# Kernel tuning notes

Measured on AMD Instinct MI355X. Metric: run time of the kernel, lower is better.

The kernel has to match this reference:

```python
import jax, jax.numpy as jnp
import numpy as np

N_NODES = 50000
N_EDGES = 800000
D = 64           # node feature / hidden dim for all 5 GCN layers
NUM_GRAPHS = 512
FINAL_NEURON = 128
OUT_DIM = 1
NUM_LAYERS = 5


def setup_inputs() -> dict:
    key = jax.random.key(0)
    ks = jax.random.split(key, 20)
    inp = {}
    inp["x"] = jax.random.normal(ks[0], (N_NODES, D), dtype=jnp.float32)
    inp["edge_index"] = jax.random.randint(ks[1], (2, N_EDGES), 0, N_NODES)
    inp["batch"] = jnp.sort(jax.random.randint(ks[2], (N_NODES,), 0, NUM_GRAPHS))
    # GCNConv weights (Glorot-ish) and biases for 5 layers, all D->D
    for i in range(NUM_LAYERS):
        inp[f"W{i+1}"] = jax.random.normal(ks[3 + i], (D, D), dtype=jnp.float32) / np.sqrt(D)
        inp[f"b{i+1}"] = jnp.zeros((D,), dtype=jnp.float32)
    inp["fc1_W"] = jax.random.normal(ks[10], (D, FINAL_NEURON), dtype=jnp.float32) / np.sqrt(D)
    inp["fc1_b"] = jnp.zeros((FINAL_NEURON,), dtype=jnp.float32)
    inp["fc2_W"] = jax.random.normal(ks[11], (FINAL_NEURON, OUT_DIM), dtype=jnp.float32) / np.sqrt(FINAL_NEURON)
    inp["fc2_b"] = jnp.zeros((OUT_DIM,), dtype=jnp.float32)
    return inp


def _gcn_conv(h, src, dst, dinv, W, b):
    # PyG GCNConv: x' = D^{-1/2} (A + I) D^{-1/2} (h W) + b, deg includes self-loop
    hw = h @ W                                           # [N, D_out]
    norm_e = dinv[src] * dinv[dst]                       # [E]
    msg = hw[src] * norm_e[:, None]                      # gather + scale
    agg = jax.ops.segment_sum(msg, dst, num_segments=h.shape[0])
    agg = agg + (dinv * dinv)[:, None] * hw              # self-loop contribution
    return agg + b


def reference(x, edge_index, batch, W1, b1, W2, b2, W3, b3, W4, b4, W5, b5,
              fc1_W, fc1_b, fc2_W, fc2_b):
    src, dst = edge_index[0], edge_index[1]
    n = x.shape[0]
    # degree on A + I (in-degree at dst, plus 1 self-loop)
    deg = jax.ops.segment_sum(jnp.ones(src.shape[0], x.dtype), dst, num_segments=n) + 1.0
    dinv = jax.lax.rsqrt(deg)
    h = x
    for W, b in ((W1, b1), (W2, b2), (W3, b3), (W4, b4), (W5, b5)):
        h = jax.nn.relu(_gcn_conv(h, src, dst, dinv, W, b))
    # global_add_pool readout over graph ids
    g = jax.ops.segment_sum(h, batch, num_segments=NUM_GRAPHS)   # [G, D]
    g = jax.nn.relu(g @ fc1_W + fc1_b)
    return g @ fc2_W + fc2_b                                     # [G, 1]
```

## Files before the change

kernel.cpp:

```cpp
#include <hip/hip_runtime.h>
#include <hip/hip_fp16.h>

#define N_NODES 50000
#define N_EDGES 800000
#define D 64
#define NUM_GRAPHS 512
#define FINAL_NEURON 128
#define SCAN_NB ((N_NODES + 255) / 256)

#define BN 16
#define NB_GEMM (N_NODES / BN)
#define NB_EDGE ((N_EDGES + 255) / 256)
#define ZS 72
#define WS 72
#define WELEM (D * WS)

typedef unsigned short ushort_t;
typedef _Float16 f16;
typedef __attribute__((ext_vector_type(4))) _Float16 f16x4;
typedef __attribute__((ext_vector_type(8))) _Float16 f16x8;
typedef __attribute__((ext_vector_type(4))) float f32x4;

struct WPtrs { const float* w[5]; };

__device__ __forceinline__ float2 h2f(unsigned v) {
    __half2 h = *reinterpret_cast<__half2*>(&v);
    return __half22float2(h);
}

__device__ __forceinline__ void acc_add8(float4& a0, float4& a1, uint4 u) {
    float2 p;
    p = h2f(u.x); a0.x += p.x; a0.y += p.y;
    p = h2f(u.y); a0.z += p.x; a0.w += p.y;
    p = h2f(u.z); a1.x += p.x; a1.y += p.y;
    p = h2f(u.w); a1.z += p.x; a1.w += p.y;
}

__global__ void k_zero_prep(int* cnt, WPtrs wp, f16* __restrict__ whi, f16* __restrict__ wlo) {
    int b = blockIdx.x;
    if (b < SCAN_NB) {
        int i = b * 256 + threadIdx.x;
        if (i < N_NODES) cnt[i] = 0;
        return;
    }
    int l = b - SCAN_NB;
    const float* W = wp.w[l];
    f16* hi = whi + l * WELEM;
    f16* lo = wlo + l * WELEM;
    for (int idx = threadIdx.x; idx < D * D; idx += 256) {
        int k = idx >> 6, j = idx & 63;
        float w = W[idx];
        f16 h = (f16)w;
        hi[j * WS + k] = h;
        lo[j * WS + k] = (f16)(w - (float)h);
    }
}

__global__ void k_hist(const int* __restrict__ dst, int* cnt, ushort_t* __restrict__ epos) {
    int e = blockIdx.x * blockDim.x + threadIdx.x;
    if (e < N_EDGES) epos[e] = (ushort_t)atomicAdd(&cnt[dst[e]], 1);
}

__global__ void k_blocksum(const int* __restrict__ cnt, int* __restrict__ bsum,
                           float* __restrict__ dinv, float* __restrict__ g) {
    __shared__ int sdata[256];
    int t = threadIdx.x;
    int i = blockIdx.x * 256 + t;
    int v = (i < N_NODES) ? cnt[i] : 0;
    if (i < N_NODES) dinv[i] = rsqrtf((float)v + 1.0f);
    if (i < NUM_GRAPHS * D) g[i] = 0.f;
    sdata[t] = v;
    __syncthreads();
    for (int s = 128; s > 0; s >>= 1) {
        if (t < s) sdata[t] += sdata[t + s];
        __syncthreads();
    }
    if (t == 0) bsum[blockIdx.x] = sdata[0];
}

__global__ void k_scanbsum(const int* __restrict__ bsum, int* __restrict__ boff) {
    __shared__ int buf[256];
    int t = threadIdx.x;
    int v = (t < SCAN_NB) ? bsum[t] : 0;
    buf[t] = v;
    __syncthreads();
    for (int off = 1; off < 256; off <<= 1) {
        int a = (t >= off) ? buf[t - off] : 0;
        __syncthreads();
        buf[t] += a;
        __syncthreads();
    }
    if (t < SCAN_NB) boff[t] = buf[t] - v;
}

__global__ void k_localscan(const int* __restrict__ cnt, const int* __restrict__ boff,
                            int* __restrict__ row) {
    __shared__ int buf[256];
    int t = threadIdx.x;
    int i = blockIdx.x * 256 + t;
    int v = (i < N_NODES) ? cnt[i] : 0;
    buf[t] = v;
    __syncthreads();
    for (int off = 1; off < 256; off <<= 1) {
        int a = (t >= off) ? buf[t - off] : 0;
        __syncthreads();
        buf[t] += a;
        __syncthreads();
    }
    if (i < N_NODES) row[i] = boff[blockIdx.x] + buf[t] - v;
    if (i == 0) row[N_NODES] = N_EDGES;
}

__device__ __forceinline__ void stage_w_lds(const f16* __restrict__ whi_g,
                                            const f16* __restrict__ wlo_g,
                                            f16* WhiT, f16* WloT, int t) {
    const uint4* sh = (const uint4*)whi_g;
    const uint4* sl = (const uint4*)wlo_g;
    uint4* dh = (uint4*)WhiT;
    uint4* dl = (uint4*)WloT;
#pragma unroll 3
    for (int i = 0; i < 3; ++i) {
        int idx = t + i * 256;
        if (idx < WELEM / 8) { dh[idx] = sh[idx]; dl[idx] = sl[idx]; }
    }
}

__device__ __forceinline__ void gather_node16(const int* __restrict__ row,
                                              const ushort_t* __restrict__ esrc,
                                              const uint4* __restrict__ hp,
                                              int n, int g, int q, float4& a0, float4& a1) {
    int e = row[n] + g, e1 = row[n + 1];
    if (g == 0) acc_add8(a0, a1, hp[(size_t)n * 8 + q]);
    int i0 = __builtin_nontemporal_load(esrc + e);
    int i1 = __builtin_nontemporal_load(esrc + e + 2);
    int i2 = __builtin_nontemporal_load(esrc + e + 4);
    int i3 = __builtin_nontemporal_load(esrc + e + 6);
    while (e + 6 < e1) {
        uint4 u0 = hp[(size_t)i0 * 8 + q];
        uint4 u1 = hp[(size_t)i1 * 8 + q];
        uint4 u2 = hp[(size_t)i2 * 8 + q];
        uint4 u3 = hp[(size_t)i3 * 8 + q];
        e += 8;
        i0 = __builtin_nontemporal_load(esrc + e);
        i1 = __builtin_nontemporal_load(esrc + e + 2);
        i2 = __builtin_nontemporal_load(esrc + e + 4);
        i3 = __builtin_nontemporal_load(esrc + e + 6);
        acc_add8(a0, a1, u0); acc_add8(a0, a1, u1);
        acc_add8(a0, a1, u2); acc_add8(a0, a1, u3);
    }
    for (; e < e1; e += 2) {
        int s = __builtin_nontemporal_load(esrc + e);
        acc_add8(a0, a1, hp[(size_t)s * 8 + q]);
    }
}

__device__ __forceinline__ void gemm_16x64(f16* zsh, const f16* WhiT, const f16* WloT,
                                           const float* dinvsh, int t) {
    int w = t >> 6, l = t & 63;
    int cb = w * 16;
    int lr = l & 15, lg = l >> 4;
    f32x4 acc = {0.f, 0.f, 0.f, 0.f};
    f16x8 a0  = *(const f16x8*)&zsh[lr * ZS + lg * 8];
    f16x8 a1  = *(const f16x8*)&zsh[lr * ZS + 32 + lg * 8];
    f16x8 bh0 = *(const f16x8*)&WhiT[(cb + lr) * WS + lg * 8];
    f16x8 bl0 = *(const f16x8*)&WloT[(cb + lr) * WS + lg * 8];
    f16x8 bh1 = *(const f16x8*)&WhiT[(cb + lr) * WS + 32 + lg * 8];
    f16x8 bl1 = *(const f16x8*)&WloT[(cb + lr) * WS + 32 + lg * 8];
    acc = __builtin_amdgcn_mfma_f32_16x16x32_f16(a0, bh0, acc, 0, 0, 0);
    acc = __builtin_amdgcn_mfma_f32_16x16x32_f16(a0, bl0, acc, 0, 0, 0);
    acc = __builtin_amdgcn_mfma_f32_16x16x32_f16(a1, bh1, acc, 0, 0, 0);
    acc = __builtin_amdgcn_mfma_f32_16x16x32_f16(a1, bl1, acc, 0, 0, 0);
    __syncthreads();
#pragma unroll
    for (int r = 0; r < 4; ++r) {
        int rrow = lg * 4 + r;
        float s = dinvsh[rrow];
        zsh[rrow * ZS + cb + lr] = (f16)(acc[r] * s);
    }
}

__global__ __launch_bounds__(256, 6)
void k_transform0(const float* __restrict__ x, const float* __restrict__ dinv,
                  const f16* __restrict__ whi_g, const f16* __restrict__ wlo_g,
                  __half* __restrict__ hout,
                  const int* __restrict__ src, const int* __restrict__ dst,
                  const int* __restrict__ row, const ushort_t* __restrict__ epos,
                  ushort_t* __restrict__ esrc) {
    int t = threadIdx.x;
    if (blockIdx.x >= NB_GEMM) {
        int e = (blockIdx.x - NB_GEMM) * 256 + t;
        if (e < N_EDGES) esrc[row[dst[e]] + (int)epos[e]] = (ushort_t)src[e];
        return;
    }
    __shared__ __attribute__((aligned(16))) f16 WhiT[WELEM];
    __shared__ __attribute__((aligned(16))) f16 WloT[WELEM];
    __shared__ __attribute__((aligned(16))) f16 zsh[BN * ZS];
    __shared__ float dinvsh[BN];
    int base = blockIdx.x * BN;
    stage_w_lds(whi_g, wlo_g, WhiT, WloT, t);
    if (t < BN) dinvsh[t] = dinv[base + t];

    int nl = t >> 4, c4 = t & 15;
    float4 xv = ((const float4*)x)[(size_t)(base + nl) * 16 + c4];
    f16x4 zv = {(f16)xv.x, (f16)xv.y, (f16)xv.z, (f16)xv.w};
    *(f16x4*)&zsh[nl * ZS + c4 * 4] = zv;
    __syncthreads();
    gemm_16x64(zsh, WhiT, WloT, dinvsh, t);
    __syncthreads();
    if (t < 128) {
        int n2 = t >> 3, q = t & 7;
        uint4 o = *(const uint4*)&zsh[n2 * ZS + q * 8];
        ((uint4*)hout)[(size_t)(base + n2) * 8 + q] = o;
    }
}

__global__ __launch_bounds__(256, 6)
void k_layer(const int* __restrict__ row, const ushort_t* __restrict__ esrc,
             const __half* __restrict__ hin, const float* __restrict__ dinv,
             const float* __restrict__ bias,
             const f16* __restrict__ whi_g, const f16* __restrict__ wlo_g,
             __half* __restrict__ hout) {
    __shared__ __attribute__((aligned(16))) f16 WhiT[WELEM];
    __shared__ __attribute__((aligned(16))) f16 WloT[WELEM];
    __shared__ __attribute__((aligned(16))) f16 zsh[BN * ZS];
    __shared__ float dinvsh[BN];
    int t = threadIdx.x;
    int base = blockIdx.x * BN;
    stage_w_lds(whi_g, wlo_g, WhiT, WloT, t);
    if (t < BN) dinvsh[t] = dinv[base + t];

    int nl = t >> 4, m = t & 15, g = m >> 3, q = m & 7;
    int n = base + nl;
    float4 a0 = {0,0,0,0}, a1 = {0,0,0,0};
    gather_node16(row, esrc, (const uint4*)hin, n, g, q, a0, a1);
    a0.x += __shfl_xor(a0.x, 8); a0.y += __shfl_xor(a0.y, 8);
    a0.z += __shfl_xor(a0.z, 8); a0.w += __shfl_xor(a0.w, 8);
    a1.x += __shfl_xor(a1.x, 8); a1.y += __shfl_xor(a1.y, 8);
    a1.z += __shfl_xor(a1.z, 8); a1.w += __shfl_xor(a1.w, 8);
    float s = dinv[n];
    float4 b0 = ((const float4*)bias)[2 * q];
    float4 b1 = ((const float4*)bias)[2 * q + 1];
    if (g == 0) {
        f16x8 zv;
        zv[0] = (f16)fmaxf(a0.x * s + b0.x, 0.f);
        zv[1] = (f16)fmaxf(a0.y * s + b0.y, 0.f);
        zv[2] = (f16)fmaxf(a0.z * s + b0.z, 0.f);
        zv[3] = (f16)fmaxf(a0.w * s + b0.w, 0.f);
        zv[4] = (f16)fmaxf(a1.x * s + b1.x, 0.f);
        zv[5] = (f16)fmaxf(a1.y * s + b1.y, 0.f);
        zv[6] = (f16)fmaxf(a1.z * s + b1.z, 0.f);
        zv[7] = (f16)fmaxf(a1.w * s + b1.w, 0.f);
        *(f16x8*)&zsh[nl * ZS + q * 8] = zv;
    }
    __syncthreads();
    gemm_16x64(zsh, WhiT, WloT, dinvsh, t);
    __syncthreads();
    if (t < 128) {
        int n2 = t >> 3, q2 = t & 7;
        uint4 o = *(const uint4*)&zsh[n2 * ZS + q2 * 8];
        ((uint4*)hout)[(size_t)(base + n2) * 8 + q2] = o;
    }
}

__global__ __launch_bounds__(256, 6)
void k_layer_pool(const int* __restrict__ row, const ushort_t* __restrict__ esrc,
                  const __half* __restrict__ hin, const float* __restrict__ dinv,
                  const float* __restrict__ bias, const int* __restrict__ batch,
                  float* __restrict__ g) {
    __shared__ float zf[BN * 68];
    __shared__ int bsh[BN];
    int t = threadIdx.x;
    int base = blockIdx.x * BN;
    if (t < BN) bsh[t] = batch[base + t];

    int nl = t >> 4, m = t & 15, g2 = m >> 3, q = m & 7;
    int n = base + nl;
    float4 a0 = {0,0,0,0}, a1 = {0,0,0,0};
    gather_node16(row, esrc, (const uint4*)hin, n, g2, q, a0, a1);
    a0.x += __shfl_xor(a0.x, 8); a0.y += __shfl_xor(a0.y, 8);
    a0.z += __shfl_xor(a0.z, 8); a0.w += __shfl_xor(a0.w, 8);
    a1.x += __shfl_xor(a1.x, 8); a1.y += __shfl_xor(a1.y, 8);
    a1.z += __shfl_xor(a1.z, 8); a1.w += __shfl_xor(a1.w, 8);
    float s = dinv[n];
    float4 b0 = ((const float4*)bias)[2 * q];
    float4 b1 = ((const float4*)bias)[2 * q + 1];
    if (g2 == 0) {
        float4 r0, r1;
        r0.x = fmaxf(a0.x * s + b0.x, 0.f);
        r0.y = fmaxf(a0.y * s + b0.y, 0.f);
        r0.z = fmaxf(a0.z * s + b0.z, 0.f);
        r0.w = fmaxf(a0.w * s + b0.w, 0.f);
        r1.x = fmaxf(a1.x * s + b1.x, 0.f);
        r1.y = fmaxf(a1.y * s + b1.y, 0.f);
        r1.z = fmaxf(a1.z * s + b1.z, 0.f);
        r1.w = fmaxf(a1.w * s + b1.w, 0.f);
        *(float4*)&zf[nl * 68 + q * 8]     = r0;
        *(float4*)&zf[nl * 68 + q * 8 + 4] = r1;
    }
    __syncthreads();
    int f = t & 63, grp = t >> 6;
    int n0 = grp * 4;
    int cur = bsh[n0];
    float acc = 0.f;
#pragma unroll
    for (int k2 = 0; k2 < 4; ++k2) {
        int bb = bsh[n0 + k2];
        if (bb != cur) { atomicAdd(&g[cur * D + f], acc); acc = 0.f; cur = bb; }
        acc += zf[(n0 + k2) * 68 + f];
    }
    atomicAdd(&g[cur * D + f], acc);
}

__global__ void k_mlp(const float* __restrict__ g, const float* __restrict__ W1,
                      const float* __restrict__ b1, const float* __restrict__ W2,
                      const float* __restrict__ b2, float* __restrict__ out) {
    __shared__ float red[FINAL_NEURON];
    int row = blockIdx.x;
    int j = threadIdx.x;
    float acc = 0.f;
#pragma unroll
    for (int k = 0; k < D; ++k) acc += g[row * D + k] * W1[k * FINAL_NEURON + j];
    acc = fmaxf(acc + b1[j], 0.f);
    red[j] = acc * W2[j];
    __syncthreads();
    for (int s = 64; s > 0; s >>= 1) {
        if (j < s) red[j] += red[j + s];
        __syncthreads();
    }
    if (j == 0) out[row] = red[0] + b2[0];
}

extern "C" void kernel_launch(void* const* d_in, const int* in_sizes, int n_in,
                              void* d_out, int out_size, void* d_ws, size_t ws_size,
                              hipStream_t stream) {
    const float* x     = (const float*)d_in[0];
    const int*   ei    = (const int*)d_in[1];
    const int*   src   = ei;
    const int*   dst   = ei + N_EDGES;
    const int*   batch = (const int*)d_in[2];
    WPtrs wp;
    wp.w[0] = (const float*)d_in[3];  wp.w[1] = (const float*)d_in[5];
    wp.w[2] = (const float*)d_in[7];  wp.w[3] = (const float*)d_in[9];
    wp.w[4] = (const float*)d_in[11];
    const float* b[5]  = {(const float*)d_in[4], (const float*)d_in[6], (const float*)d_in[8],
                          (const float*)d_in[10], (const float*)d_in[12]};
    const float* fc1W  = (const float*)d_in[13];
    const float* fc1b  = (const float*)d_in[14];
    const float* fc2W  = (const float*)d_in[15];
    const float* fc2b  = (const float*)d_in[16];
    float* out = (float*)d_out;

    __half*   yA   = (__half*)d_ws;
    __half*   yB   = yA + (size_t)N_NODES * D;
    f16*      whiG = (f16*)(yB + (size_t)N_NODES * D);
    f16*      wloG = whiG + 5 * WELEM;
    float*    g    = (float*)(wloG + 5 * WELEM);
    float*    dinv = g + NUM_GRAPHS * D;
    int*      cnt  = (int*)(dinv + N_NODES);
    int*      row  = cnt + N_NODES;
    int*      bsum = row + N_NODES + 1;
    int*      boff = bsum + 256;
    ushort_t* epos = (ushort_t*)(boff + 256);
    ushort_t* esrc = epos + N_EDGES;

    k_zero_prep<<<SCAN_NB + 5, 256, 0, stream>>>(cnt, wp, whiG, wloG);
    k_hist<<<(N_EDGES + 255) / 256, 256, 0, stream>>>(dst, cnt, epos);
    k_blocksum<<<SCAN_NB, 256, 0, stream>>>(cnt, bsum, dinv, g);
    k_scanbsum<<<1, 256, 0, stream>>>(bsum, boff);
    k_localscan<<<SCAN_NB, 256, 0, stream>>>(cnt, boff, row);

    k_transform0<<<NB_GEMM + NB_EDGE, 256, 0, stream>>>(x, dinv, whiG, wloG, yA,
                                                        src, dst, row, epos, esrc);

    k_layer<<<NB_GEMM, 256, 0, stream>>>(row, esrc, yA, dinv, b[0],
                                         whiG + 1 * WELEM, wloG + 1 * WELEM, yB);
    k_layer<<<NB_GEMM, 256, 0, stream>>>(row, esrc, yB, dinv, b[1],
                                         whiG + 2 * WELEM, wloG + 2 * WELEM, yA);
    k_layer<<<NB_GEMM, 256, 0, stream>>>(row, esrc, yA, dinv, b[2],
                                         whiG + 3 * WELEM, wloG + 3 * WELEM, yB);
    k_layer<<<NB_GEMM, 256, 0, stream>>>(row, esrc, yB, dinv, b[3],
                                         whiG + 4 * WELEM, wloG + 4 * WELEM, yA);

    k_layer_pool<<<NB_GEMM, 256, 0, stream>>>(row, esrc, yA, dinv, b[4], batch, g);

    k_mlp<<<NUM_GRAPHS, FINAL_NEURON, 0, stream>>>(g, fc1W, fc1b, fc2W, fc2b, out);
}
```

Baseline: 262.8 us.

## Fuse transform, GCN layers, pooling and MLP into one cooperative persistent kernel

Merges the edge-scatter/first transform, four layer kernels, the pooled last layer and the MLP head into a single cooperative kernel. Blocks loop over tiles persistently and use grid-wide syncs between stages, replacing seven kernel launches and their inter-kernel gaps. Each block stages a layer's weights into LDS once per layer instead of once per tile. The trade-offs are grid-sync cost, a grid capped by occupancy (256 CUs assumed), and LDS reuse across stages. The edge scatter now runs before the transform inside the same blocks rather than in parallel blocks.

```diff
diff --git a/kernel.cpp b/kernel.cpp
--- a/kernel.cpp
+++ b/kernel.cpp
@@ -1,5 +1,8 @@
 #include <hip/hip_runtime.h>
 #include <hip/hip_fp16.h>
+#include <hip/hip_cooperative_groups.h>
+
+namespace cg = cooperative_groups;
 
 #define N_NODES 50000
 #define N_EDGES 800000
@@ -10,7 +13,7 @@
 
 #define BN 16
 #define NB_GEMM (N_NODES / BN)
-#define NB_EDGE ((N_EDGES + 255) / 256)
+#define NB_EDGE (N_EDGES / 256)
 #define ZS 72
 #define WS 72
 #define WELEM (D * WS)
@@ -22,6 +25,19 @@
 typedef __attribute__((ext_vector_type(4))) float f32x4;
 
 struct WPtrs { const float* w[5]; };
+
+struct MegaArgs {
+    const float* x;
+    const int* src; const int* dst; const int* batch;
+    const int* row; const ushort_t* epos; ushort_t* esrc;
+    const float* dinv;
+    const f16* whi[5]; const f16* wlo[5];
+    const float* bias[5];
+    __half* yA; __half* yB;
+    float* g;
+    const float* fc1W; const float* fc1b; const float* fc2W; const float* fc2b;
+    float* out;
+};
 
 __device__ __forceinline__ float2 h2f(unsigned v) {
     __half2 h = *reinterpret_cast<__half2*>(&v);
@@ -180,154 +196,152 @@
 }
 
 __global__ __launch_bounds__(256, 6)
-void k_transform0(const float* __restrict__ x, const float* __restrict__ dinv,
-                  const f16* __restrict__ whi_g, const f16* __restrict__ wlo_g,
-                  __half* __restrict__ hout,
-                  const int* __restrict__ src, const int* __restrict__ dst,
-                  const int* __restrict__ row, const ushort_t* __restrict__ epos,
-                  ushort_t* __restrict__ esrc) {
-    int t = threadIdx.x;
-    if (blockIdx.x >= NB_GEMM) {
-        int e = (blockIdx.x - NB_GEMM) * 256 + t;
-        if (e < N_EDGES) esrc[row[dst[e]] + (int)epos[e]] = (ushort_t)src[e];
-        return;
-    }
-    __shared__ __attribute__((aligned(16))) f16 WhiT[WELEM];
-    __shared__ __attribute__((aligned(16))) f16 WloT[WELEM];
-    __shared__ __attribute__((aligned(16))) f16 zsh[BN * ZS];
-    __shared__ float dinvsh[BN];
-    int base = blockIdx.x * BN;
-    stage_w_lds(whi_g, wlo_g, WhiT, WloT, t);
-    if (t < BN) dinvsh[t] = dinv[base + t];
-
-    int nl = t >> 4, c4 = t & 15;
-    float4 xv = ((const float4*)x)[(size_t)(base + nl) * 16 + c4];
-    f16x4 zv = {(f16)xv.x, (f16)xv.y, (f16)xv.z, (f16)xv.w};
-    *(f16x4*)&zsh[nl * ZS + c4 * 4] = zv;
-    __syncthreads();
-    gemm_16x64(zsh, WhiT, WloT, dinvsh, t);
-    __syncthreads();
-    if (t < 128) {
-        int n2 = t >> 3, q = t & 7;
-        uint4 o = *(const uint4*)&zsh[n2 * ZS + q * 8];
-        ((uint4*)hout)[(size_t)(base + n2) * 8 + q] = o;
-    }
-}
-
-__global__ __launch_bounds__(256, 6)
-void k_layer(const int* __restrict__ row, const ushort_t* __restrict__ esrc,
-             const __half* __restrict__ hin, const float* __restrict__ dinv,
-             const float* __restrict__ bias,
-             const f16* __restrict__ whi_g, const f16* __restrict__ wlo_g,
-             __half* __restrict__ hout) {
+void k_mega(MegaArgs A) {
+    cg::grid_group gridg = cg::this_grid();
     __shared__ __attribute__((aligned(16))) f16 WhiT[WELEM];
     __shared__ __attribute__((aligned(16))) f16 WloT[WELEM];
     __shared__ __attribute__((aligned(16))) f16 zsh[BN * ZS];
     __shared__ float dinvsh[BN];
     int t = threadIdx.x;
-    int base = blockIdx.x * BN;
-    stage_w_lds(whi_g, wlo_g, WhiT, WloT, t);
-    if (t < BN) dinvsh[t] = dinv[base + t];
-
-    int nl = t >> 4, m = t & 15, g = m >> 3, q = m & 7;
-    int n = base + nl;
-    float4 a0 = {0,0,0,0}, a1 = {0,0,0,0};
-    gather_node16(row, esrc, (const uint4*)hin, n, g, q, a0, a1);
-    a0.x += __shfl_xor(a0.x, 8); a0.y += __shfl_xor(a0.y, 8);
-    a0.z += __shfl_xor(a0.z, 8); a0.w += __shfl_xor(a0.w, 8);
-    a1.x += __shfl_xor(a1.x, 8); a1.y += __shfl_xor(a1.y, 8);
-    a1.z += __shfl_xor(a1.z, 8); a1.w += __shfl_xor(a1.w, 8);
-    float s = dinv[n];
-    float4 b0 = ((const float4*)bias)[2 * q];
-    float4 b1 = ((const float4*)bias)[2 * q + 1];
-    if (g == 0) {
-        f16x8 zv;
-        zv[0] = (f16)fmaxf(a0.x * s + b0.x, 0.f);
-        zv[1] = (f16)fmaxf(a0.y * s + b0.y, 0.f);
-        zv[2] = (f16)fmaxf(a0.z * s + b0.z, 0.f);
-        zv[3] = (f16)fmaxf(a0.w * s + b0.w, 0.f);
-        zv[4] = (f16)fmaxf(a1.x * s + b1.x, 0.f);
-        zv[5] = (f16)fmaxf(a1.y * s + b1.y, 0.f);
-        zv[6] = (f16)fmaxf(a1.z * s + b1.z, 0.f);
-        zv[7] = (f16)fmaxf(a1.w * s + b1.w, 0.f);
-        *(f16x8*)&zsh[nl * ZS + q * 8] = zv;
-    }
+    const int nblk = gridDim.x;
+
+    for (int c = blockIdx.x; c < NB_EDGE; c += nblk) {
+        int e = c * 256 + t;
+        A.esrc[A.row[A.dst[e]] + (int)A.epos[e]] = (ushort_t)A.src[e];
+    }
+    stage_w_lds(A.whi[0], A.wlo[0], WhiT, WloT, t);
     __syncthreads();
-    gemm_16x64(zsh, WhiT, WloT, dinvsh, t);
-    __syncthreads();
-    if (t < 128) {
-        int n2 = t >> 3, q2 = t & 7;
-        uint4 o = *(const uint4*)&zsh[n2 * ZS + q2 * 8];
-        ((uint4*)hout)[(size_t)(base + n2) * 8 + q2] = o;
-    }
-}
-
-__global__ __launch_bounds__(256, 6)
-void k_layer_pool(const int* __restrict__ row, const ushort_t* __restrict__ esrc,
-                  const __half* __restrict__ hin, const float* __restrict__ dinv,
-                  const float* __restrict__ bias, const int* __restrict__ batch,
-                  float* __restrict__ g) {
-    __shared__ float zf[BN * 68];
-    __shared__ int bsh[BN];
-    int t = threadIdx.x;
-    int base = blockIdx.x * BN;
-    if (t < BN) bsh[t] = batch[base + t];
-
-    int nl = t >> 4, m = t & 15, g2 = m >> 3, q = m & 7;
-    int n = base + nl;
-    float4 a0 = {0,0,0,0}, a1 = {0,0,0,0};
-    gather_node16(row, esrc, (const uint4*)hin, n, g2, q, a0, a1);
-    a0.x += __shfl_xor(a0.x, 8); a0.y += __shfl_xor(a0.y, 8);
-    a0.z += __shfl_xor(a0.z, 8); a0.w += __shfl_xor(a0.w, 8);
-    a1.x += __shfl_xor(a1.x, 8); a1.y += __shfl_xor(a1.y, 8);
-    a1.z += __shfl_xor(a1.z, 8); a1.w += __shfl_xor(a1.w, 8);
-    float s = dinv[n];
-    float4 b0 = ((const float4*)bias)[2 * q];
-    float4 b1 = ((const float4*)bias)[2 * q + 1];
-    if (g2 == 0) {
-        float4 r0, r1;
-        r0.x = fmaxf(a0.x * s + b0.x, 0.f);
-        r0.y = fmaxf(a0.y * s + b0.y, 0.f);
-        r0.z = fmaxf(a0.z * s + b0.z, 0.f);
-        r0.w = fmaxf(a0.w * s + b0.w, 0.f);
-        r1.x = fmaxf(a1.x * s + b1.x, 0.f);
-        r1.y = fmaxf(a1.y * s + b1.y, 0.f);
-        r1.z = fmaxf(a1.z * s + b1.z, 0.f);
-        r1.w = fmaxf(a1.w * s + b1.w, 0.f);
-        *(float4*)&zf[nl * 68 + q * 8]     = r0;
-        *(float4*)&zf[nl * 68 + q * 8 + 4] = r1;
-    }
-    __syncthreads();
-    int f = t & 63, grp = t >> 6;
-    int n0 = grp * 4;
-    int cur = bsh[n0];
-    float acc = 0.f;
+    for (int tile = blockIdx.x; tile < NB_GEMM; tile += nblk) {
+        int base = tile * BN;
+        if (t < BN) dinvsh[t] = A.dinv[base + t];
+        int nl = t >> 4, c4 = t & 15;
+        float4 xv = ((const float4*)A.x)[(size_t)(base + nl) * 16 + c4];
+        f16x4 zv = {(f16)xv.x, (f16)xv.y, (f16)xv.z, (f16)xv.w};
+        *(f16x4*)&zsh[nl * ZS + c4 * 4] = zv;
+        __syncthreads();
+        gemm_16x64(zsh, WhiT, WloT, dinvsh, t);
+        __syncthreads();
+        if (t < 128) {
+            int n2 = t >> 3, q = t & 7;
+            uint4 o = *(const uint4*)&zsh[n2 * ZS + q * 8];
+            ((uint4*)A.yA)[(size_t)(base + n2) * 8 + q] = o;
+        }
+        __syncthreads();
+    }
+    gridg.sync();
+
+    const __half* hin = A.yA;
+    __half* hout = A.yB;
+    for (int l = 0; l < 4; ++l) {
+        stage_w_lds(A.whi[l + 1], A.wlo[l + 1], WhiT, WloT, t);
+        __syncthreads();
+        const float* bias = A.bias[l];
+        for (int tile = blockIdx.x; tile < NB_GEMM; tile += nblk) {
+            int base = tile * BN;
+            if (t < BN) dinvsh[t] = A.dinv[base + t];
+            int nl = t >> 4, m = t & 15, g = m >> 3, q = m & 7;
+            int n = base + nl;
+            float4 a0 = {0,0,0,0}, a1 = {0,0,0,0};
+            gather_node16(A.row, A.esrc, (const uint4*)hin, n, g, q, a0, a1);
+            a0.x += __shfl_xor(a0.x, 8); a0.y += __shfl_xor(a0.y, 8);
+            a0.z += __shfl_xor(a0.z, 8); a0.w += __shfl_xor(a0.w, 8);
+            a1.x += __shfl_xor(a1.x, 8); a1.y += __shfl_xor(a1.y, 8);
+            a1.z += __shfl_xor(a1.z, 8); a1.w += __shfl_xor(a1.w, 8);
+            float s = A.dinv[n];
+            float4 b0 = ((const float4*)bias)[2 * q];
+            float4 b1 = ((const float4*)bias)[2 * q + 1];
+            if (g == 0) {
+                f16x8 zv;
+                zv[0] = (f16)fmaxf(a0.x * s + b0.x, 0.f);
+                zv[1] = (f16)fmaxf(a0.y * s + b0.y, 0.f);
+                zv[2] = (f16)fmaxf(a0.z * s + b0.z, 0.f);
+                zv[3] = (f16)fmaxf(a0.w * s + b0.w, 0.f);
+                zv[4] = (f16)fmaxf(a1.x * s + b1.x, 0.f);
+                zv[5] = (f16)fmaxf(a1.y * s + b1.y, 0.f);
+                zv[6] = (f16)fmaxf(a1.z * s + b1.z, 0.f);
+                zv[7] = (f16)fmaxf(a1.w * s + b1.w, 0.f);
+                *(f16x8*)&zsh[nl * ZS + q * 8] = zv;
+            }
+            __syncthreads();
+            gemm_16x64(zsh, WhiT, WloT, dinvsh, t);
+            __syncthreads();
+            if (t < 128) {
+                int n2 = t >> 3, q2 = t & 7;
+                uint4 o = *(const uint4*)&zsh[n2 * ZS + q2 * 8];
+                ((uint4*)hout)[(size_t)(base + n2) * 8 + q2] = o;
+            }
+            __syncthreads();
+        }
+        gridg.sync();
+        __half* tmp = (__half*)hin; hin = hout; hout = tmp;
+    }
+
+    {
+        float* zf = (float*)WhiT;
+        int*   bsh = (int*)WloT;
+        const float* bias = A.bias[4];
+        for (int tile = blockIdx.x; tile < NB_GEMM; tile += nblk) {
+            int base = tile * BN;
+            if (t < BN) bsh[t] = A.batch[base + t];
+            int nl = t >> 4, m = t & 15, g2 = m >> 3, q = m & 7;
+            int n = base + nl;
+            float4 a0 = {0,0,0,0}, a1 = {0,0,0,0};
+            gather_node16(A.row, A.esrc, (const uint4*)hin, n, g2, q, a0, a1);
+            a0.x += __shfl_xor(a0.x, 8); a0.y += __shfl_xor(a0.y, 8);
+            a0.z += __shfl_xor(a0.z, 8); a0.w += __shfl_xor(a0.w, 8);
+            a1.x += __shfl_xor(a1.x, 8); a1.y += __shfl_xor(a1.y, 8);
+            a1.z += __shfl_xor(a1.z, 8); a1.w += __shfl_xor(a1.w, 8);
+            float s = A.dinv[n];
+            float4 b0 = ((const float4*)bias)[2 * q];
+            float4 b1 = ((const float4*)bias)[2 * q + 1];
+            if (g2 == 0) {
+                float4 r0, r1;
+                r0.x = fmaxf(a0.x * s + b0.x, 0.f);
+                r0.y = fmaxf(a0.y * s + b0.y, 0.f);
+                r0.z = fmaxf(a0.z * s + b0.z, 0.f);
+                r0.w = fmaxf(a0.w * s + b0.w, 0.f);
+                r1.x = fmaxf(a1.x * s + b1.x, 0.f);
+                r1.y = fmaxf(a1.y * s + b1.y, 0.f);
+                r1.z = fmaxf(a1.z * s + b1.z, 0.f);
+                r1.w = fmaxf(a1.w * s + b1.w, 0.f);
+                *(float4*)&zf[nl * 68 + q * 8]     = r0;
+                *(float4*)&zf[nl * 68 + q * 8 + 4] = r1;
+            }
+            __syncthreads();
+            int f = t & 63, grp = t >> 6;
+            int n0 = grp * 4;
+            int cur = bsh[n0];
+            float acc = 0.f;
 #pragma unroll
-    for (int k2 = 0; k2 < 4; ++k2) {
-        int bb = bsh[n0 + k2];
-        if (bb != cur) { atomicAdd(&g[cur * D + f], acc); acc = 0.f; cur = bb; }
-        acc += zf[(n0 + k2) * 68 + f];
-    }
-    atomicAdd(&g[cur * D + f], acc);
-}
-
-__global__ void k_mlp(const float* __restrict__ g, const float* __restrict__ W1,
-                      const float* __restrict__ b1, const float* __restrict__ W2,
-                      const float* __restrict__ b2, float* __restrict__ out) {
-    __shared__ float red[FINAL_NEURON];
-    int row = blockIdx.x;
-    int j = threadIdx.x;
-    float acc = 0.f;
+            for (int k2 = 0; k2 < 4; ++k2) {
+                int bb = bsh[n0 + k2];
+                if (bb != cur) { atomicAdd(&A.g[cur * D + f], acc); acc = 0.f; cur = bb; }
+                acc += zf[(n0 + k2) * 68 + f];
+            }
+            atomicAdd(&A.g[cur * D + f], acc);
+            __syncthreads();
+        }
+    }
+    gridg.sync();
+
+    if (blockIdx.x < NUM_GRAPHS) {
+        float* red = (float*)zsh;
+        int rowi = blockIdx.x;
+        float acc = 0.f;
+        if (t < FINAL_NEURON) {
 #pragma unroll
-    for (int k = 0; k < D; ++k) acc += g[row * D + k] * W1[k * FINAL_NEURON + j];
-    acc = fmaxf(acc + b1[j], 0.f);
-    red[j] = acc * W2[j];
-    __syncthreads();
-    for (int s = 64; s > 0; s >>= 1) {
-        if (j < s) red[j] += red[j + s];
-        __syncthreads();
-    }
-    if (j == 0) out[row] = red[0] + b2[0];
+            for (int k = 0; k < D; ++k)
+                acc += A.g[rowi * D + k] * A.fc1W[k * FINAL_NEURON + t];
+            acc = fmaxf(acc + A.fc1b[t], 0.f);
+            red[t] = acc * A.fc2W[t];
+        }
+        __syncthreads();
+        for (int s = 64; s > 0; s >>= 1) {
+            if (t < s) red[t] += red[t + s];
+            __syncthreads();
+        }
+        if (t == 0) A.out[rowi] = red[0] + A.fc2b[0];
+    }
 }
 
 extern "C" void kernel_launch(void* const* d_in, const int* in_sizes, int n_in,
@@ -344,10 +358,6 @@
     wp.w[4] = (const float*)d_in[11];
     const float* b[5]  = {(const float*)d_in[4], (const float*)d_in[6], (const float*)d_in[8],
                           (const float*)d_in[10], (const float*)d_in[12]};
-    const float* fc1W  = (const float*)d_in[13];
-    const float* fc1b  = (const float*)d_in[14];
-    const float* fc2W  = (const float*)d_in[15];
-    const float* fc2b  = (const float*)d_in[16];
     float* out = (float*)d_out;
 
     __half*   yA   = (__half*)d_ws;
@@ -369,19 +379,27 @@
     k_scanbsum<<<1, 256, 0, stream>>>(bsum, boff);
     k_localscan<<<SCAN_NB, 256, 0, stream>>>(cnt, boff, row);
 
-    k_transform0<<<NB_GEMM + NB_EDGE, 256, 0, stream>>>(x, dinv, whiG, wloG, yA,
-                                                        src, dst, row, epos, esrc);
-
-    k_layer<<<NB_GEMM, 256, 0, stream>>>(row, esrc, yA, dinv, b[0],
-                                         whiG + 1 * WELEM, wloG + 1 * WELEM, yB);
-    k_layer<<<NB_GEMM, 256, 0, stream>>>(row, esrc, yB, dinv, b[1],
-                                         whiG + 2 * WELEM, wloG + 2 * WELEM, yA);
-    k_layer<<<NB_GEMM, 256, 0, stream>>>(row, esrc, yA, dinv, b[2],
-                                         whiG + 3 * WELEM, wloG + 3 * WELEM, yB);
-    k_layer<<<NB_GEMM, 256, 0, stream>>>(row, esrc, yB, dinv, b[3],
-                                         whiG + 4 * WELEM, wloG + 4 * WELEM, yA);
-
-    k_layer_pool<<<NB_GEMM, 256, 0, stream>>>(row, esrc, yA, dinv, b[4], batch, g);
-
-    k_mlp<<<NUM_GRAPHS, FINAL_NEURON, 0, stream>>>(g, fc1W, fc1b, fc2W, fc2b, out);
-}
+    MegaArgs A;
+    A.x = x; A.src = src; A.dst = dst; A.batch = batch;
+    A.row = row; A.epos = epos; A.esrc = esrc; A.dinv = dinv;
+    for (int l = 0; l < 5; ++l) {
+        A.whi[l] = whiG + l * WELEM;
+        A.wlo[l] = wloG + l * WELEM;
+        A.bias[l] = b[l];
+    }
+    A.yA = yA; A.yB = yB; A.g = g;
+    A.fc1W = (const float*)d_in[13]; A.fc1b = (const float*)d_in[14];
+    A.fc2W = (const float*)d_in[15]; A.fc2b = (const float*)d_in[16];
+    A.out = out;
+
+    static int gblocks = 0;
+    if (gblocks == 0) {
+        int nb = 0;
+        hipError_t err = hipOccupancyMaxActiveBlocksPerMultiprocessor(&nb, k_mega, 256, 0);
+        if (err != hipSuccess || nb < 1) nb = 4;
+        gblocks = nb * 256;
+        if (gblocks > NB_GEMM) gblocks = NB_GEMM;
+    }
+    void* kp[] = { (void*)&A };
+    hipLaunchCooperativeKernel(k_mega, dim3(gblocks), dim3(256), kp, 0, stream);
+}
```

After: 883.1 us. 3.36x slower.

## Split node features into two 32-wide planes and separate gather from GEMM

Applied to the files above, without the earlier changes.

Node features are stored as two feature-half planes, so each gather pass reads 64-byte rows from a smaller working set that fits better in cache. Each plane gets its own gather blocks. The fused gather+GEMM layer kernel is split into a gather kernel, which writes a scaled aggregate to a new fp16 buffer, and an apply kernel, which adds bias, applies ReLU and runs the MFMA GEMM. This costs an extra kernel launch per layer, an extra write and read of the aggregate, another fp16 rounding step, and reading each edge index list twice (once per plane).

```diff
diff --git a/kernel.cpp b/kernel.cpp
--- a/kernel.cpp
+++ b/kernel.cpp
@@ -10,10 +10,14 @@
 
 #define BN 16
 #define NB_GEMM (N_NODES / BN)
-#define NB_EDGE ((N_EDGES + 255) / 256)
+#define NB_EDGE (N_EDGES / 256)
+#define BG 32
+#define NB_GATH (((N_NODES + BG - 1) / BG) * 2)
 #define ZS 72
 #define WS 72
 #define WELEM (D * WS)
+
+#define PLANE_U4 ((size_t)N_NODES * 4)
 
 typedef unsigned short ushort_t;
 typedef _Float16 f16;
@@ -125,21 +129,22 @@
     }
 }
 
-__device__ __forceinline__ void gather_node16(const int* __restrict__ row,
-                                              const ushort_t* __restrict__ esrc,
-                                              const uint4* __restrict__ hp,
-                                              int n, int g, int q, float4& a0, float4& a1) {
-    int e = row[n] + g, e1 = row[n + 1];
-    if (g == 0) acc_add8(a0, a1, hp[(size_t)n * 8 + q]);
+__device__ __forceinline__ void gather_plane(const int* __restrict__ row,
+                                             const ushort_t* __restrict__ esrc,
+                                             const uint4* __restrict__ hp,
+                                             int n, int grp, int q,
+                                             float4& a0, float4& a1) {
+    int e = row[n] + grp, e1 = row[n + 1];
+    if (grp == 0) acc_add8(a0, a1, hp[(size_t)n * 4 + q]);
     int i0 = __builtin_nontemporal_load(esrc + e);
     int i1 = __builtin_nontemporal_load(esrc + e + 2);
     int i2 = __builtin_nontemporal_load(esrc + e + 4);
     int i3 = __builtin_nontemporal_load(esrc + e + 6);
     while (e + 6 < e1) {
-        uint4 u0 = hp[(size_t)i0 * 8 + q];
-        uint4 u1 = hp[(size_t)i1 * 8 + q];
-        uint4 u2 = hp[(size_t)i2 * 8 + q];
-        uint4 u3 = hp[(size_t)i3 * 8 + q];
+        uint4 u0 = hp[(size_t)i0 * 4 + q];
+        uint4 u1 = hp[(size_t)i1 * 4 + q];
+        uint4 u2 = hp[(size_t)i2 * 4 + q];
+        uint4 u3 = hp[(size_t)i3 * 4 + q];
         e += 8;
         i0 = __builtin_nontemporal_load(esrc + e);
         i1 = __builtin_nontemporal_load(esrc + e + 2);
@@ -150,7 +155,7 @@
     }
     for (; e < e1; e += 2) {
         int s = __builtin_nontemporal_load(esrc + e);
-        acc_add8(a0, a1, hp[(size_t)s * 8 + q]);
+        acc_add8(a0, a1, hp[(size_t)s * 4 + q]);
     }
 }
 
@@ -208,18 +213,44 @@
     gemm_16x64(zsh, WhiT, WloT, dinvsh, t);
     __syncthreads();
     if (t < 128) {
-        int n2 = t >> 3, q = t & 7;
-        uint4 o = *(const uint4*)&zsh[n2 * ZS + q * 8];
-        ((uint4*)hout)[(size_t)(base + n2) * 8 + q] = o;
+        int n2 = t >> 3, c = t & 7;
+        uint4 o = *(const uint4*)&zsh[n2 * ZS + c * 8];
+        ((uint4*)hout)[(size_t)(c >> 2) * PLANE_U4 + (size_t)(base + n2) * 4 + (c & 3)] = o;
+    }
+}
+
+__global__ __launch_bounds__(256, 8)
+void k_gatherp(const int* __restrict__ row, const ushort_t* __restrict__ esrc,
+               const __half* __restrict__ hin, const float* __restrict__ dinv,
+               __half* __restrict__ agg) {
+    int t = threadIdx.x;
+    int p = blockIdx.x & 1;
+    int n = (blockIdx.x >> 1) * BG + (t >> 3);
+    if (n >= N_NODES) return;
+    int m = t & 7, grp = m >> 2, q = m & 3;
+    const uint4* hp = (const uint4*)hin + (size_t)p * PLANE_U4;
+    float4 a0 = {0,0,0,0}, a1 = {0,0,0,0};
+    gather_plane(row, esrc, hp, n, grp, q, a0, a1);
+    a0.x += __shfl_xor(a0.x, 4); a0.y += __shfl_xor(a0.y, 4);
+    a0.z += __shfl_xor(a0.z, 4); a0.w += __shfl_xor(a0.w, 4);
+    a1.x += __shfl_xor(a1.x, 4); a1.y += __shfl_xor(a1.y, 4);
+    a1.z += __shfl_xor(a1.z, 4); a1.w += __shfl_xor(a1.w, 4);
+    if (grp == 0) {
+        float s = dinv[n];
+        __half2 q0 = __floats2half2_rn(a0.x * s, a0.y * s);
+        __half2 q1 = __floats2half2_rn(a0.z * s, a0.w * s);
+        __half2 q2 = __floats2half2_rn(a1.x * s, a1.y * s);
+        __half2 q3 = __floats2half2_rn(a1.z * s, a1.w * s);
+        uint4 pk = {*(unsigned*)&q0, *(unsigned*)&q1, *(unsigned*)&q2, *(unsigned*)&q3};
+        ((uint4*)agg)[(size_t)p * PLANE_U4 + (size_t)n * 4 + q] = pk;
     }
 }
 
 __global__ __launch_bounds__(256, 6)
-void k_layer(const int* __restrict__ row, const ushort_t* __restrict__ esrc,
-             const __half* __restrict__ hin, const float* __restrict__ dinv,
-             const float* __restrict__ bias,
-             const f16* __restrict__ whi_g, const f16* __restrict__ wlo_g,
-             __half* __restrict__ hout) {
+void k_applyp(const __half* __restrict__ agg, const float* __restrict__ dinv,
+              const float* __restrict__ bias,
+              const f16* __restrict__ whi_g, const f16* __restrict__ wlo_g,
+              __half* __restrict__ hout) {
     __shared__ __attribute__((aligned(16))) f16 WhiT[WELEM];
     __shared__ __attribute__((aligned(16))) f16 WloT[WELEM];
     __shared__ __attribute__((aligned(16))) f16 zsh[BN * ZS];
@@ -228,87 +259,80 @@
     int base = blockIdx.x * BN;
     stage_w_lds(whi_g, wlo_g, WhiT, WloT, t);
     if (t < BN) dinvsh[t] = dinv[base + t];
-
-    int nl = t >> 4, m = t & 15, g = m >> 3, q = m & 7;
+    if (t < 128) {
+        int nl = t >> 3, c = t & 7;
+        uint4 u = ((const uint4*)agg)[(size_t)(c >> 2) * PLANE_U4 +
+                                      (size_t)(base + nl) * 4 + (c & 3)];
+        float4 b0 = ((const float4*)bias)[2 * c];
+        float4 b1 = ((const float4*)bias)[2 * c + 1];
+        float2 pp;
+        f16x8 zv;
+        pp = h2f(u.x); zv[0] = (f16)fmaxf(pp.x + b0.x, 0.f); zv[1] = (f16)fmaxf(pp.y + b0.y, 0.f);
+        pp = h2f(u.y); zv[2] = (f16)fmaxf(pp.x + b0.z, 0.f); zv[3] = (f16)fmaxf(pp.y + b0.w, 0.f);
+        pp = h2f(u.z); zv[4] = (f16)fmaxf(pp.x + b1.x, 0.f); zv[5] = (f16)fmaxf(pp.y + b1.y, 0.f);
+        pp = h2f(u.w); zv[6] = (f16)fmaxf(pp.x + b1.z, 0.f); zv[7] = (f16)fmaxf(pp.y + b1.w, 0.f);
+        *(f16x8*)&zsh[nl * ZS + c * 8] = zv;
+    }
+    __syncthreads();
+    gemm_16x64(zsh, WhiT, WloT, dinvsh, t);
+    __syncthreads();
+    if (t < 128) {
+        int n2 = t >> 3, c = t & 7;
+        uint4 o = *(const uint4*)&zsh[n2 * ZS + c * 8];
+        ((uint4*)hout)[(size_t)(c >> 2) * PLANE_U4 + (size_t)(base + n2) * 4 + (c & 3)] = o;
+    }
+}
+
+__global__ __launch_bounds__(256, 8)
+void k_gather_pool(const int* __restrict__ row, const ushort_t* __restrict__ esrc,
+                   const __half* __restrict__ hin, const float* __restrict__ dinv,
+                   const float* __restrict__ bias, const int* __restrict__ batch,
+                   float* __restrict__ g) {
+    __shared__ float zf[BG][36];
+    __shared__ int bsh[BG];
+    int t = threadIdx.x;
+    int p = blockIdx.x & 1;
+    int base = (blockIdx.x >> 1) * BG;
+    if (t < BG) bsh[t] = (base + t < N_NODES) ? batch[base + t] : -1;
+    int nl = t >> 3, m = t & 7, grp = m >> 2, q = m & 3;
     int n = base + nl;
     float4 a0 = {0,0,0,0}, a1 = {0,0,0,0};
-    gather_node16(row, esrc, (const uint4*)hin, n, g, q, a0, a1);
-    a0.x += __shfl_xor(a0.x, 8); a0.y += __shfl_xor(a0.y, 8);
-    a0.z += __shfl_xor(a0.z, 8); a0.w += __shfl_xor(a0.w, 8);
-    a1.x += __shfl_xor(a1.x, 8); a1.y += __shfl_xor(a1.y, 8);
-    a1.z += __shfl_xor(a1.z, 8); a1.w += __shfl_xor(a1.w, 8);
-    float s = dinv[n];
-    float4 b0 = ((const float4*)bias)[2 * q];
-    float4 b1 = ((const float4*)bias)[2 * q + 1];
-    if (g == 0) {
-        f16x8 zv;
-        zv[0] = (f16)fmaxf(a0.x * s + b0.x, 0.f);
-        zv[1] = (f16)fmaxf(a0.y * s + b0.y, 0.f);
-        zv[2] = (f16)fmaxf(a0.z * s + b0.z, 0.f);
-        zv[3] = (f16)fmaxf(a0.w * s + b0.w, 0.f);
-        zv[4] = (f16)fmaxf(a1.x * s + b1.x, 0.f);
-        zv[5] = (f16)fmaxf(a1.y * s + b1.y, 0.f);
-        zv[6] = (f16)fmaxf(a1.z * s + b1.z, 0.f);
-        zv[7] = (f16)fmaxf(a1.w * s + b1.w, 0.f);
-        *(f16x8*)&zsh[nl * ZS + q * 8] = zv;
-    }
-    __syncthreads();
-    gemm_16x64(zsh, WhiT, WloT, dinvsh, t);
-    __syncthreads();
-    if (t < 128) {
-        int n2 = t >> 3, q2 = t & 7;
-        uint4 o = *(const uint4*)&zsh[n2 * ZS + q2 * 8];
-        ((uint4*)hout)[(size_t)(base + n2) * 8 + q2] = o;
-    }
-}
-
-__global__ __launch_bounds__(256, 6)
-void k_layer_pool(const int* __restrict__ row, const ushort_t* __restrict__ esrc,
-                  const __half* __restrict__ hin, const float* __restrict__ dinv,
-                  const float* __restrict__ bias, const int* __restrict__ batch,
-                  float* __restrict__ g) {
-    __shared__ float zf[BN * 68];
-    __shared__ int bsh[BN];
-    int t = threadIdx.x;
-    int base = blockIdx.x * BN;
-    if (t < BN) bsh[t] = batch[base + t];
-
-    int nl = t >> 4, m = t & 15, g2 = m >> 3, q = m & 7;
-    int n = base + nl;
-    float4 a0 = {0,0,0,0}, a1 = {0,0,0,0};
-    gather_node16(row, esrc, (const uint4*)hin, n, g2, q, a0, a1);
-    a0.x += __shfl_xor(a0.x, 8); a0.y += __shfl_xor(a0.y, 8);
-    a0.z += __shfl_xor(a0.z, 8); a0.w += __shfl_xor(a0.w, 8);
-    a1.x += __shfl_xor(a1.x, 8); a1.y += __shfl_xor(a1.y, 8);
-    a1.z += __shfl_xor(a1.z, 8); a1.w += __shfl_xor(a1.w, 8);
-    float s = dinv[n];
-    float4 b0 = ((const float4*)bias)[2 * q];
-    float4 b1 = ((const float4*)bias)[2 * q + 1];
-    if (g2 == 0) {
-        float4 r0, r1;
-        r0.x = fmaxf(a0.x * s + b0.x, 0.f);
-        r0.y = fmaxf(a0.y * s + b0.y, 0.f);
-        r0.z = fmaxf(a0.z * s + b0.z, 0.f);
-        r0.w = fmaxf(a0.w * s + b0.w, 0.f);
-        r1.x = fmaxf(a1.x * s + b1.x, 0.f);
-        r1.y = fmaxf(a1.y * s + b1.y, 0.f);
-        r1.z = fmaxf(a1.z * s + b1.z, 0.f);
-        r1.w = fmaxf(a1.w * s + b1.w, 0.f);
-        *(float4*)&zf[nl * 68 + q * 8]     = r0;
-        *(float4*)&zf[nl * 68 + q * 8 + 4] = r1;
-    }
-    __syncthreads();
-    int f = t & 63, grp = t >> 6;
-    int n0 = grp * 4;
+    float s = 0.f;
+    if (n < N_NODES) {
+        const uint4* hp = (const uint4*)hin + (size_t)p * PLANE_U4;
+        gather_plane(row, esrc, hp, n, grp, q, a0, a1);
+        s = dinv[n];
+    }
+    a0.x += __shfl_xor(a0.x, 4); a0.y += __shfl_xor(a0.y, 4);
+    a0.z += __shfl_xor(a0.z, 4); a0.w += __shfl_xor(a0.w, 4);
+    a1.x += __shfl_xor(a1.x, 4); a1.y += __shfl_xor(a1.y, 4);
+    a1.z += __shfl_xor(a1.z, 4); a1.w += __shfl_xor(a1.w, 4);
+    if (grp == 0) {
+        float4 b0 = ((const float4*)bias)[p * 8 + 2 * q];
+        float4 b1 = ((const float4*)bias)[p * 8 + 2 * q + 1];
+        float* zr = &zf[nl][q * 8];
+        zr[0] = fmaxf(a0.x * s + b0.x, 0.f);
+        zr[1] = fmaxf(a0.y * s + b0.y, 0.f);
+        zr[2] = fmaxf(a0.z * s + b0.z, 0.f);
+        zr[3] = fmaxf(a0.w * s + b0.w, 0.f);
+        zr[4] = fmaxf(a1.x * s + b1.x, 0.f);
+        zr[5] = fmaxf(a1.y * s + b1.y, 0.f);
+        zr[6] = fmaxf(a1.z * s + b1.z, 0.f);
+        zr[7] = fmaxf(a1.w * s + b1.w, 0.f);
+    }
+    __syncthreads();
+    int f = t & 31, gg = t >> 5;
+    int n0 = gg * 4;
     int cur = bsh[n0];
     float acc = 0.f;
 #pragma unroll
     for (int k2 = 0; k2 < 4; ++k2) {
         int bb = bsh[n0 + k2];
-        if (bb != cur) { atomicAdd(&g[cur * D + f], acc); acc = 0.f; cur = bb; }
-        acc += zf[(n0 + k2) * 68 + f];
-    }
-    atomicAdd(&g[cur * D + f], acc);
+        if (bb < 0) break;
+        if (bb != cur) { atomicAdd(&g[cur * D + p * 32 + f], acc); acc = 0.f; cur = bb; }
+        acc += zf[n0 + k2][f];
+    }
+    if (cur >= 0) atomicAdd(&g[cur * D + p * 32 + f], acc);
 }
 
 __global__ void k_mlp(const float* __restrict__ g, const float* __restrict__ W1,
@@ -352,7 +376,8 @@
 
     __half*   yA   = (__half*)d_ws;
     __half*   yB   = yA + (size_t)N_NODES * D;
-    f16*      whiG = (f16*)(yB + (size_t)N_NODES * D);
+    __half*   agg  = yB + (size_t)N_NODES * D;
+    f16*      whiG = (f16*)(agg + (size_t)N_NODES * D);
     f16*      wloG = whiG + 5 * WELEM;
     float*    g    = (float*)(wloG + 5 * WELEM);
     float*    dinv = g + NUM_GRAPHS * D;
@@ -372,16 +397,20 @@
     k_transform0<<<NB_GEMM + NB_EDGE, 256, 0, stream>>>(x, dinv, whiG, wloG, yA,
                                                         src, dst, row, epos, esrc);
 
-    k_layer<<<NB_GEMM, 256, 0, stream>>>(row, esrc, yA, dinv, b[0],
-                                         whiG + 1 * WELEM, wloG + 1 * WELEM, yB);
-    k_layer<<<NB_GEMM, 256, 0, stream>>>(row, esrc, yB, dinv, b[1],
-                                         whiG + 2 * WELEM, wloG + 2 * WELEM, yA);
-    k_layer<<<NB_GEMM, 256, 0, stream>>>(row, esrc, yA, dinv, b[2],
-                                         whiG + 3 * WELEM, wloG + 3 * WELEM, yB);
-    k_layer<<<NB_GEMM, 256, 0, stream>>>(row, esrc, yB, dinv, b[3],
-                                         whiG + 4 * WELEM, wloG + 4 * WELEM, yA);
-
-    k_layer_pool<<<NB_GEMM, 256, 0, stream>>>(row, esrc, yA, dinv, b[4], batch, g);
+    k_gatherp<<<NB_GATH, 256, 0, stream>>>(row, esrc, yA, dinv, agg);
+    k_applyp <<<NB_GEMM, 256, 0, stream>>>(agg, dinv, b[0],
+                                           whiG + 1 * WELEM, wloG + 1 * WELEM, yB);
+    k_gatherp<<<NB_GATH, 256, 0, stream>>>(row, esrc, yB, dinv, agg);
+    k_applyp <<<NB_GEMM, 256, 0, stream>>>(agg, dinv, b[1],
+                                           whiG + 2 * WELEM, wloG + 2 * WELEM, yA);
+    k_gatherp<<<NB_GATH, 256, 0, stream>>>(row, esrc, yA, dinv, agg);
+    k_applyp <<<NB_GEMM, 256, 0, stream>>>(agg, dinv, b[2],
+                                           whiG + 3 * WELEM, wloG + 3 * WELEM, yB);
+    k_gatherp<<<NB_GATH, 256, 0, stream>>>(row, esrc, yB, dinv, agg);
+    k_applyp <<<NB_GEMM, 256, 0, stream>>>(agg, dinv, b[3],
+                                           whiG + 4 * WELEM, wloG + 4 * WELEM, yA);
+
+    k_gather_pool<<<NB_GATH, 256, 0, stream>>>(row, esrc, yA, dinv, b[4], batch, g);
 
     k_mlp<<<NUM_GRAPHS, FINAL_NEURON, 0, stream>>>(g, fc1W, fc1b, fc2W, fc2b, out);
 }
```

Result: slower. 299.5 us (+14.0%).
